# Kernel tuning notes

Measured on AMD Instinct MI355X. Metric: run time of the kernel, lower is better.

The kernel has to match this reference:

```python
import jax, jax.numpy as jnp
import numpy as np

N_EST = 5      # n_estimators
DEPTH = 6      # n_depth
LEAVES = 64    # 2 ** n_depth


def setup_inputs() -> dict:
    key = jax.random.key(0)
    ks = jax.random.split(key, 6)
    N, F, H, L, O = 131072, 256, 384, 64, 16
    X = jax.random.normal(ks[0], (N, F), jnp.float32)
    W1 = jax.random.normal(ks[1], (F, H), jnp.float32) / np.float32(np.sqrt(F))
    b1 = jnp.zeros((H,), jnp.float32)
    W2 = jax.random.normal(ks[2], (H, L), jnp.float32) / np.float32(np.sqrt(H))
    b2 = jnp.zeros((L,), jnp.float32)
    # phi[i] = random choice of n_leaves indices from arange(n_latent) without replacement
    phi = jnp.stack([jax.random.permutation(jax.random.fold_in(ks[3], i), L)[:LEAVES]
                     for i in range(N_EST)]).astype(jnp.int32)  # [E, 64]
    # pi: per-estimator leaf->label distributions (rows on the simplex, as after softmax updates)
    pi = jax.nn.softmax(jax.random.normal(ks[4], (N_EST, LEAVES, O), jnp.float32), axis=-1)
    return {"X": X, "W1": W1, "b1": b1, "W2": W2, "b2": b2, "phi": phi, "pi": pi}


def reference(X, W1, b1, W2, b2, phi, pi):
    # Backbone MLP: sigmoid -> sigmoid, as in keras.Sequential([Dense(h,'sigmoid'), Dense(l,'sigmoid')])
    h = jax.nn.sigmoid(X @ W1 + b1)          # [N, H]
    latent = jax.nn.sigmoid(h @ W2 + b2)     # [N, L]

    N = X.shape[0]
    E = phi.shape[0]
    d = latent[:, phi]                        # gather per estimator -> [N, E, 64]
    decisions = jnp.stack([d, 1.0 - d], axis=-1)  # [N, E, 64, 2] (go-left / go-right probs)

    # Soft tree routing: product of decision probs along each root->leaf path.
    # Level `lev` uses node indices [begin:begin+2**lev); index 0 is unused (matches TF code).
    mu = jnp.ones((N, E, 1, 1), X.dtype)
    begin = 1
    for lev in range(DEPTH):
        end = begin + 2 ** lev
        # reshape [N,E,k,2] -> [N,E,2k,1]; broadcast against [N,E,k_level,2] replaces tile(1,1,2)
        mu = mu.reshape(N, E, -1, 1) * decisions[:, :, begin:end, :]
        begin = end
    mu = mu.reshape(N, E, LEAVES)             # [N, E, 64] leaf arrival probabilities

    # predict: mean over estimators of mu_e @ pi_e
    return jnp.einsum('nel,elo->no', mu, pi) / E
```

## Files before the change

kernel.cpp:

```cpp
#include <hip/hip_runtime.h>
#include <hip/hip_bf16.h>
#include <stdint.h>

#define F_DIM 256
#define H_DIM 384
#define L_DIM 64
#define O_DIM 16
#define E_NUM 5
#define BM 64

#define XK_STRIDE 264
#define H_STRIDE 392
#define LAT_STRIDE 65
#define MU_STRIDE 328

#define LATT_OFF 50176
#define PHIS_OFF 66816
#define SMEM_BYTES 68096

typedef short bf16x8 __attribute__((ext_vector_type(8)));
typedef float f32x4 __attribute__((ext_vector_type(4)));

__device__ __forceinline__ unsigned short f2bf(float f) {
    union { float f; unsigned int u; } v; v.f = f;
    unsigned int u = v.u;
    return (unsigned short)((u + 0x7FFFu + ((u >> 16) & 1u)) >> 16);
}

__device__ __forceinline__ unsigned int pk2(float a, float b) {
#if defined(__has_builtin)
#if __has_builtin(__builtin_amdgcn_cvt_pk_bf16_f32)
    typedef __bf16 bf2 __attribute__((ext_vector_type(2)));
    bf2 p = __builtin_amdgcn_cvt_pk_bf16_f32(a, b);
    union { bf2 v; unsigned int u; } c; c.v = p;
    return c.u;
#else
    return (unsigned int)f2bf(a) | ((unsigned int)f2bf(b) << 16);
#endif
#else
    return (unsigned int)f2bf(a) | ((unsigned int)f2bf(b) << 16);
#endif
}

__device__ __forceinline__ uint2 cvt4(float4 v) {
    uint2 r; r.x = pk2(v.x, v.y); r.y = pk2(v.z, v.w); return r;
}

__device__ __forceinline__ float sigmoidf(float x) {
    return __builtin_amdgcn_rcpf(1.0f + __builtin_amdgcn_exp2f(-1.44269504088896f * x));
}

__global__ void prep_kernel(const float* __restrict__ W1, const float* __restrict__ W2,
                            const float* __restrict__ pi,
                            unsigned short* __restrict__ W1f,
                            unsigned short* __restrict__ W2f,
                            unsigned short* __restrict__ piTf) {
    __shared__ float tile[32][33];
    const int b = blockIdx.x;
    const int tid = threadIdx.x;
    const int tx = tid & 31, ty = tid >> 5;

    if (b < 120) {
        int ks, t0, nks;
        unsigned short* dst;
        if (b < 96) {
            const int fb = b / 12, hb = b % 12;
            #pragma unroll
            for (int s = 0; s < 32; s += 8)
                tile[ty + s][tx] = W1[(size_t)(fb * 32 + ty + s) * H_DIM + hb * 32 + tx];
            ks = fb; t0 = hb * 2; nks = 8; dst = W1f;
        } else {
            const int bb = b - 96, hb = bb / 2, lb = bb % 2;
            #pragma unroll
            for (int s = 0; s < 32; s += 8)
                tile[ty + s][tx] = W2[(size_t)(hb * 32 + ty + s) * L_DIM + lb * 32 + tx];
            ks = hb; t0 = lb * 2; nks = 12; dst = W2f;
        }
        __syncthreads();
        const int t_local = tid >> 7;
        const int r = (tid * 2) & 255;
        const int lane = r >> 2;
        const int e2b = r & 3;
        const int q = lane >> 4, c = lane & 15;
        const int f0 = q * 8 + e2b * 2;
        const int hl = t_local * 16 + c;
        uint2 v;
        v.x = pk2(tile[f0 + 0][hl], tile[f0 + 1][hl]);
        v.y = pk2(tile[f0 + 2][hl], tile[f0 + 3][hl]);
        const size_t off = ((size_t)((t0 + t_local) * nks + ks) * 64 + lane) * 8 + e2b * 2;
        *(uint2*)(dst + off) = v;
    } else {
        for (int i = tid; i < O_DIM * E_NUM * L_DIM; i += 256) {
            const int j = i & 7, lane = (i >> 3) & 63, ks = i >> 9;
            const int q = lane >> 4, c = lane & 15;
            const int k = ks * 32 + q * 8 + j;
            piTf[i] = f2bf(pi[k * O_DIM + c] * 0.2f);
        }
    }
}

__global__ __launch_bounds__(512, 4) void fused_kernel(
    const float* __restrict__ X,
    const unsigned short* __restrict__ W1f,
    const float* __restrict__ b1,
    const unsigned short* __restrict__ W2f,
    const float* __restrict__ b2,
    const int* __restrict__ phi,
    const unsigned short* __restrict__ piTf,
    float* __restrict__ out) {

    __shared__ __align__(16) unsigned char smem[SMEM_BYTES];
    unsigned short* Xs  = (unsigned short*)smem;
    unsigned short* Hs  = (unsigned short*)smem;
    unsigned short* mus = (unsigned short*)smem;
    float*          latT = (float*)(smem + LATT_OFF);
    int*            phis = (int*)(smem + PHIS_OFF);

    if (blockIdx.x < 512 && ((blockIdx.x >> 8) & 1)) {
        __builtin_amdgcn_s_sleep(127);
    }

    const int tid  = threadIdx.x;
    const int wave = tid >> 6;
    const int lane = tid & 63;
    const int q    = lane >> 4;
    const int c    = lane & 15;
    const int row0 = blockIdx.x * BM;

    if (tid < E_NUM * L_DIM) phis[tid] = phi[tid];

    {
        float4 t0[8];
        #pragma unroll
        for (int i = 0; i < 8; ++i)
            t0[i] = *(const float4*)(X + (size_t)(row0 + wave * 8 + i) * F_DIM + lane * 4);
        #pragma unroll
        for (int i = 0; i < 8; ++i)
            *(uint2*)&Xs[(wave * 8 + i) * XK_STRIDE + lane * 4] = cvt4(t0[i]);
    }

    bf16x8 af0[3];
    #pragma unroll
    for (int i = 0; i < 3; ++i)
        af0[i] = *(const bf16x8*)(W1f + ((size_t)((wave * 3 + i) * 8 + 0) * 64 + lane) * 8);

    __syncthreads();

    f32x4 acc[3][4];
    #pragma unroll
    for (int i = 0; i < 3; ++i)
        #pragma unroll
        for (int j = 0; j < 4; ++j)
            acc[i][j] = (f32x4){0.f, 0.f, 0.f, 0.f};

    {
        bf16x8 bf0[4];
        #pragma unroll
        for (int j = 0; j < 4; ++j)
            bf0[j] = *(const bf16x8*)&Xs[(j * 16 + c) * XK_STRIDE + q * 8];
        #pragma unroll
        for (int i = 0; i < 3; ++i)
            #pragma unroll
            for (int j = 0; j < 4; ++j)
                acc[i][j] = __builtin_amdgcn_mfma_f32_16x16x32_bf16(af0[i], bf0[j], acc[i][j], 0, 0, 0);
    }
    #pragma unroll 2
    for (int ks = 1; ks < 8; ++ks) {
        bf16x8 af[3];
        #pragma unroll
        for (int i = 0; i < 3; ++i)
            af[i] = *(const bf16x8*)(W1f + ((size_t)((wave * 3 + i) * 8 + ks) * 64 + lane) * 8);
        bf16x8 bf_[4];
        #pragma unroll
        for (int j = 0; j < 4; ++j)
            bf_[j] = *(const bf16x8*)&Xs[(j * 16 + c) * XK_STRIDE + ks * 32 + q * 8];
        #pragma unroll
        for (int i = 0; i < 3; ++i)
            #pragma unroll
            for (int j = 0; j < 4; ++j)
                acc[i][j] = __builtin_amdgcn_mfma_f32_16x16x32_bf16(af[i], bf_[j], acc[i][j], 0, 0, 0);
    }
    __syncthreads();

    const int lt = wave >> 1;
    bf16x8 wfrag[12];
    #pragma unroll
    for (int ks = 0; ks < 12; ++ks)
        wfrag[ks] = *(const bf16x8*)(W2f + ((size_t)(lt * 12 + ks) * 64 + lane) * 8);

    #pragma unroll
    for (int i = 0; i < 3; ++i) {
        const int n0 = wave * 48 + i * 16 + q * 4;
        float4 bv = *(const float4*)(b1 + n0);
        #pragma unroll
        for (int j = 0; j < 4; ++j) {
            const int m = j * 16 + c;
            uint2 h2;
            h2.x = pk2(sigmoidf(acc[i][j][0] + bv.x), sigmoidf(acc[i][j][1] + bv.y));
            h2.y = pk2(sigmoidf(acc[i][j][2] + bv.z), sigmoidf(acc[i][j][3] + bv.w));
            *(uint2*)&Hs[m * H_STRIDE + n0] = h2;
        }
    }
    __syncthreads();

    {
        const int mbase = (wave & 1) * 2;
        f32x4 acc2[2];
        acc2[0] = (f32x4){0.f, 0.f, 0.f, 0.f};
        acc2[1] = (f32x4){0.f, 0.f, 0.f, 0.f};
        #pragma unroll
        for (int ks = 0; ks < 12; ++ks) {
            #pragma unroll
            for (int j = 0; j < 2; ++j) {
                bf16x8 bf_ = *(const bf16x8*)&Hs[((mbase + j) * 16 + c) * H_STRIDE + ks * 32 + q * 8];
                acc2[j] = __builtin_amdgcn_mfma_f32_16x16x32_bf16(wfrag[ks], bf_, acc2[j], 0, 0, 0);
            }
        }
        const float4 b2v = *(const float4*)(b2 + lt * 16 + q * 4);
        #pragma unroll
        for (int j = 0; j < 2; ++j) {
            const int m = (mbase + j) * 16 + c;
            #pragma unroll
            for (int rg = 0; rg < 4; ++rg) {
                const int l = lt * 16 + q * 4 + rg;
                latT[l * LAT_STRIDE + m] = sigmoidf(acc2[j][rg] + ((const float*)&b2v)[rg]);
            }
        }
    }
    __syncthreads();

    bf16x8 pfrag[10];
    if (wave >= 5) {
        #pragma unroll
        for (int ks = 0; ks < 10; ++ks)
            pfrag[ks] = *(const bf16x8*)(piTf + ((size_t)ks * 64 + lane) * 8);
    }

    if (wave < E_NUM) {
        const int e = wave;
        const int r = lane;
        float mu[64];
        mu[0] = 1.0f;
        #pragma unroll
        for (int lev = 0; lev < 6; ++lev) {
            const int w = 1 << lev;
            #pragma unroll
            for (int i = w - 1; i >= 0; --i) {
                float d = latT[phis[e * 64 + w + i] * LAT_STRIDE + r];
                float m = mu[i];
                mu[2 * i + 1] = m - m * d;
                mu[2 * i]     = m * d;
            }
        }
        #pragma unroll
        for (int j8 = 0; j8 < 8; ++j8) {
            bf16x8 v;
            #pragma unroll
            for (int t = 0; t < 4; ++t) {
                unsigned int p = pk2(mu[j8 * 8 + 2 * t], mu[j8 * 8 + 2 * t + 1]);
                v[2 * t]     = (short)(p & 0xFFFF);
                v[2 * t + 1] = (short)(p >> 16);
            }
            *((bf16x8*)&mus[r * MU_STRIDE + e * 64 + j8 * 8]) = v;
        }
    }
    __syncthreads();

    if (wave >= 5) {
        for (int mt = wave - 5; mt < 4; mt += (wave == 5 ? 3 : 4)) {
            f32x4 acc3 = (f32x4){0.f, 0.f, 0.f, 0.f};
            #pragma unroll
            for (int ks = 0; ks < 10; ++ks) {
                bf16x8 af = *((const bf16x8*)&mus[(mt * 16 + c) * MU_STRIDE + ks * 32 + q * 8]);
                acc3 = __builtin_amdgcn_mfma_f32_16x16x32_bf16(af, pfrag[ks], acc3, 0, 0, 0);
            }
            #pragma unroll
            for (int rg = 0; rg < 4; ++rg) {
                const int m = mt * 16 + q * 4 + rg;
                out[(size_t)(row0 + m) * O_DIM + c] = acc3[rg];
            }
        }
    }
}

extern "C" void kernel_launch(void* const* d_in, const int* in_sizes, int n_in,
                              void* d_out, int out_size, void* d_ws, size_t ws_size,
                              hipStream_t stream) {
    (void)in_sizes; (void)n_in; (void)out_size; (void)ws_size;
    const float* X  = (const float*)d_in[0];
    const float* W1 = (const float*)d_in[1];
    const float* b1 = (const float*)d_in[2];
    const float* W2 = (const float*)d_in[3];
    const float* b2 = (const float*)d_in[4];
    const int*   phi = (const int*)d_in[5];
    const float* pi  = (const float*)d_in[6];
    float* out = (float*)d_out;

    unsigned short* W1f  = (unsigned short*)d_ws;
    unsigned short* W2f  = (unsigned short*)((char*)d_ws + 196608);
    unsigned short* piTf = (unsigned short*)((char*)d_ws + 196608 + 49152);

    prep_kernel<<<121, 256, 0, stream>>>(W1, W2, pi, W1f, W2f, piTf);

    const int nblocks = 131072 / BM;
    fused_kernel<<<nblocks, 512, 0, stream>>>(X, W1f, b1, W2f, b2, phi, piTf, out);
}
```

Before: 240.2 us.

## Split fused MLP-tree kernel into GEMM1 kernel and tail kernel via workspace

```diff
diff --git a/kernel.cpp b/kernel.cpp
--- a/kernel.cpp
+++ b/kernel.cpp
@@ -7,16 +7,11 @@
 #define L_DIM 64
 #define O_DIM 16
 #define E_NUM 5
-#define BM 64
 
 #define XK_STRIDE 264
 #define H_STRIDE 392
-#define LAT_STRIDE 65
-#define MU_STRIDE 328
-
-#define LATT_OFF 50176
-#define PHIS_OFF 66816
-#define SMEM_BYTES 68096
+#define LAT_STRIDE 33
+#define LAT_STRIDE64 65
 
 typedef short bf16x8 __attribute__((ext_vector_type(8)));
 typedef float f32x4 __attribute__((ext_vector_type(4)));
@@ -99,6 +94,214 @@
     }
 }
 
+__global__ __launch_bounds__(512, 4) void gemm1_kernel(
+    const float* __restrict__ X,
+    const unsigned short* __restrict__ W1f,
+    const float* __restrict__ b1,
+    unsigned short* __restrict__ Hf) {
+
+    __shared__ __align__(16) unsigned short Xs[64 * XK_STRIDE];
+
+    const int tid  = threadIdx.x;
+    const int wave = tid >> 6;
+    const int lane = tid & 63;
+    const int q    = lane >> 4;
+    const int c    = lane & 15;
+    const int row0 = blockIdx.x * 64;
+
+    {
+        float4 t0[8];
+        #pragma unroll
+        for (int i = 0; i < 8; ++i)
+            t0[i] = *(const float4*)(X + (size_t)(row0 + wave * 8 + i) * F_DIM + lane * 4);
+        #pragma unroll
+        for (int i = 0; i < 8; ++i)
+            *(uint2*)&Xs[(wave * 8 + i) * XK_STRIDE + lane * 4] = cvt4(t0[i]);
+    }
+
+    bf16x8 af0[3];
+    #pragma unroll
+    for (int i = 0; i < 3; ++i)
+        af0[i] = *(const bf16x8*)(W1f + ((size_t)((wave * 3 + i) * 8 + 0) * 64 + lane) * 8);
+
+    __syncthreads();
+
+    f32x4 acc[3][4];
+    #pragma unroll
+    for (int i = 0; i < 3; ++i)
+        #pragma unroll
+        for (int j = 0; j < 4; ++j)
+            acc[i][j] = (f32x4){0.f, 0.f, 0.f, 0.f};
+
+    {
+        bf16x8 bf0[4];
+        #pragma unroll
+        for (int j = 0; j < 4; ++j)
+            bf0[j] = *(const bf16x8*)&Xs[(j * 16 + c) * XK_STRIDE + q * 8];
+        #pragma unroll
+        for (int i = 0; i < 3; ++i)
+            #pragma unroll
+            for (int j = 0; j < 4; ++j)
+                acc[i][j] = __builtin_amdgcn_mfma_f32_16x16x32_bf16(af0[i], bf0[j], acc[i][j], 0, 0, 0);
+    }
+    #pragma unroll 2
+    for (int ks = 1; ks < 8; ++ks) {
+        bf16x8 af[3];
+        #pragma unroll
+        for (int i = 0; i < 3; ++i)
+            af[i] = *(const bf16x8*)(W1f + ((size_t)((wave * 3 + i) * 8 + ks) * 64 + lane) * 8);
+        bf16x8 bf_[4];
+        #pragma unroll
+        for (int j = 0; j < 4; ++j)
+            bf_[j] = *(const bf16x8*)&Xs[(j * 16 + c) * XK_STRIDE + ks * 32 + q * 8];
+        #pragma unroll
+        for (int i = 0; i < 3; ++i)
+            #pragma unroll
+            for (int j = 0; j < 4; ++j)
+                acc[i][j] = __builtin_amdgcn_mfma_f32_16x16x32_bf16(af[i], bf_[j], acc[i][j], 0, 0, 0);
+    }
+
+    const int mtGbase = blockIdx.x * 4;
+    #pragma unroll
+    for (int i = 0; i < 3; ++i) {
+        const int colbase = wave * 48 + i * 16 + q * 4;
+        const int ks2 = colbase >> 5;
+        const int qp  = (colbase >> 3) & 3;
+        const int jj0 = colbase & 7;
+        const float4 bv = *(const float4*)(b1 + colbase);
+        #pragma unroll
+        for (int j = 0; j < 4; ++j) {
+            uint2 h2;
+            h2.x = pk2(sigmoidf(acc[i][j][0] + bv.x), sigmoidf(acc[i][j][1] + bv.y));
+            h2.y = pk2(sigmoidf(acc[i][j][2] + bv.z), sigmoidf(acc[i][j][3] + bv.w));
+            *(uint2*)(Hf + ((size_t)((mtGbase + j) * 12 + ks2) * 64 + qp * 16 + c) * 8 + jj0) = h2;
+        }
+    }
+}
+
+__global__ __launch_bounds__(256, 4) void tail_kernel(
+    const unsigned short* __restrict__ Hf,
+    const unsigned short* __restrict__ W2f,
+    const float* __restrict__ b2,
+    const int* __restrict__ phi,
+    const unsigned short* __restrict__ piTf,
+    float* __restrict__ out) {
+
+    __shared__ __align__(16) unsigned char smem[34304];
+    unsigned short* HsL  = (unsigned short*)smem;
+    unsigned short* musf = (unsigned short*)smem;
+    float*          latT = (float*)(smem + 24576);
+    int*            phis = (int*)(smem + 33024);
+
+    const int tid  = threadIdx.x;
+    const int wave = tid >> 6;
+    const int lane = tid & 63;
+    const int q    = lane >> 4;
+    const int c    = lane & 15;
+    const int row0 = blockIdx.x * 32;
+
+    uint4 hv[6];
+    #pragma unroll
+    for (int s = 0; s < 6; ++s)
+        hv[s] = *(const uint4*)(Hf + (size_t)blockIdx.x * 12288 + s * 2048 + tid * 8);
+
+    for (int idx = tid; idx < E_NUM * L_DIM; idx += 256) phis[idx] = phi[idx];
+
+    bf16x8 wfrag[12];
+    #pragma unroll
+    for (int ks = 0; ks < 12; ++ks)
+        wfrag[ks] = *(const bf16x8*)(W2f + ((size_t)(wave * 12 + ks) * 64 + lane) * 8);
+
+    #pragma unroll
+    for (int s = 0; s < 6; ++s)
+        *(uint4*)&HsL[s * 2048 + tid * 8] = hv[s];
+
+    __syncthreads();
+
+    {
+        f32x4 acc2[2];
+        acc2[0] = (f32x4){0.f, 0.f, 0.f, 0.f};
+        acc2[1] = (f32x4){0.f, 0.f, 0.f, 0.f};
+        #pragma unroll
+        for (int ks = 0; ks < 12; ++ks) {
+            #pragma unroll
+            for (int j = 0; j < 2; ++j) {
+                bf16x8 bf_ = *(const bf16x8*)&HsL[((j * 12 + ks) * 64 + lane) * 8];
+                acc2[j] = __builtin_amdgcn_mfma_f32_16x16x32_bf16(wfrag[ks], bf_, acc2[j], 0, 0, 0);
+            }
+        }
+        const int lb = wave * 16;
+        const float4 b2v = *(const float4*)(b2 + lb + q * 4);
+        #pragma unroll
+        for (int j = 0; j < 2; ++j) {
+            const int m = j * 16 + c;
+            #pragma unroll
+            for (int rg = 0; rg < 4; ++rg) {
+                const int l = lb + q * 4 + rg;
+                latT[l * LAT_STRIDE + m] = sigmoidf(acc2[j][rg] + ((const float*)&b2v)[rg]);
+            }
+        }
+    }
+    __syncthreads();
+
+    {
+        const int r = lane & 31;
+        const int e = wave * 2 + (lane >> 5);
+        if (e < E_NUM) {
+            float mu[64];
+            mu[0] = 1.0f;
+            #pragma unroll
+            for (int lev = 0; lev < 6; ++lev) {
+                const int w = 1 << lev;
+                #pragma unroll
+                for (int i = w - 1; i >= 0; --i) {
+                    float d = latT[phis[e * 64 + w + i] * LAT_STRIDE + r];
+                    float m = mu[i];
+                    mu[2 * i + 1] = m - m * d;
+                    mu[2 * i]     = m * d;
+                }
+            }
+            const int mt = r >> 4;
+            const int rc = r & 15;
+            #pragma unroll
+            for (int j8 = 0; j8 < 8; ++j8) {
+                bf16x8 v;
+                #pragma unroll
+                for (int t = 0; t < 4; ++t) {
+                    unsigned int p = pk2(mu[j8 * 8 + 2 * t], mu[j8 * 8 + 2 * t + 1]);
+                    v[2 * t]     = (short)(p & 0xFFFF);
+                    v[2 * t + 1] = (short)(p >> 16);
+                }
+                const int ksf = 2 * e + (j8 >> 2);
+                const int qf  = j8 & 3;
+                *((bf16x8*)&musf[((mt * 10 + ksf) * 64 + qf * 16 + rc) * 8]) = v;
+            }
+        }
+    }
+    __syncthreads();
+
+    if (wave >= 2) {
+        const int mt = wave - 2;
+        bf16x8 pfrag[10];
+        #pragma unroll
+        for (int ks = 0; ks < 10; ++ks)
+            pfrag[ks] = *(const bf16x8*)(piTf + ((size_t)ks * 64 + lane) * 8);
+        f32x4 acc3 = (f32x4){0.f, 0.f, 0.f, 0.f};
+        #pragma unroll
+        for (int ks = 0; ks < 10; ++ks) {
+            bf16x8 af = *((const bf16x8*)&musf[((mt * 10 + ks) * 64 + lane) * 8]);
+            acc3 = __builtin_amdgcn_mfma_f32_16x16x32_bf16(af, pfrag[ks], acc3, 0, 0, 0);
+        }
+        #pragma unroll
+        for (int rg = 0; rg < 4; ++rg) {
+            const int m = mt * 16 + q * 4 + rg;
+            out[(size_t)(row0 + m) * O_DIM + c] = acc3[rg];
+        }
+    }
+}
+
+#define FB_LATT_OFF 50176
+#define FB_PHIS_OFF 66816
 __global__ __launch_bounds__(512, 4) void fused_kernel(
     const float* __restrict__ X,
     const unsigned short* __restrict__ W1f,
@@ -109,23 +312,20 @@
     const unsigned short* __restrict__ piTf,
     float* __restrict__ out) {
 
-    __shared__ __align__(16) unsigned char smem[SMEM_BYTES];
-    unsigned short* Xs  = (unsigned short*)smem;
-    unsigned short* Hs  = (unsigned short*)smem;
-    unsigned short* mus = (unsigned short*)smem;
-    float*          latT = (float*)(smem + LATT_OFF);
-    int*            phis = (int*)(smem + PHIS_OFF);
-
-    if (blockIdx.x < 512 && ((blockIdx.x >> 8) & 1)) {
-        __builtin_amdgcn_s_sleep(127);
-    }
+    __shared__ __align__(16) unsigned char smem[68096];
+    unsigned short* Xs   = (unsigned short*)smem;
+    unsigned short* Hs   = (unsigned short*)smem;
+    unsigned short* mus  = (unsigned short*)smem;
+    float*          latT = (float*)(smem + FB_LATT_OFF);
+    int*            phis = (int*)(smem + FB_PHIS_OFF);
+    #define MU_STRIDE 328
 
     const int tid  = threadIdx.x;
     const int wave = tid >> 6;
     const int lane = tid & 63;
     const int q    = lane >> 4;
     const int c    = lane & 15;
-    const int row0 = blockIdx.x * BM;
+    const int row0 = blockIdx.x * 64;
 
     if (tid < E_NUM * L_DIM) phis[tid] = phi[tid];
 
@@ -138,12 +338,10 @@
         for (int i = 0; i < 8; ++i)
             *(uint2*)&Xs[(wave * 8 + i) * XK_STRIDE + lane * 4] = cvt4(t0[i]);
     }
-
     bf16x8 af0[3];
     #pragma unroll
     for (int i = 0; i < 3; ++i)
         af0[i] = *(const bf16x8*)(W1f + ((size_t)((wave * 3 + i) * 8 + 0) * 64 + lane) * 8);
-
     __syncthreads();
 
     f32x4 acc[3][4];
@@ -152,7 +350,6 @@
         #pragma unroll
         for (int j = 0; j < 4; ++j)
             acc[i][j] = (f32x4){0.f, 0.f, 0.f, 0.f};
-
     {
         bf16x8 bf0[4];
         #pragma unroll
@@ -223,7 +420,7 @@
             #pragma unroll
             for (int rg = 0; rg < 4; ++rg) {
                 const int l = lt * 16 + q * 4 + rg;
-                latT[l * LAT_STRIDE + m] = sigmoidf(acc2[j][rg] + ((const float*)&b2v)[rg]);
+                latT[l * LAT_STRIDE64 + m] = sigmoidf(acc2[j][rg] + ((const float*)&b2v)[rg]);
             }
         }
     }
@@ -235,7 +432,6 @@
         for (int ks = 0; ks < 10; ++ks)
             pfrag[ks] = *(const bf16x8*)(piTf + ((size_t)ks * 64 + lane) * 8);
     }
-
     if (wave < E_NUM) {
         const int e = wave;
         const int r = lane;
@@ -246,7 +442,7 @@
             const int w = 1 << lev;
             #pragma unroll
             for (int i = w - 1; i >= 0; --i) {
-                float d = latT[phis[e * 64 + w + i] * LAT_STRIDE + r];
+                float d = latT[phis[e * 64 + w + i] * LAT_STRIDE64 + r];
                 float m = mu[i];
                 mu[2 * i + 1] = m - m * d;
                 mu[2 * i]     = m * d;
@@ -286,7 +482,7 @@
 extern "C" void kernel_launch(void* const* d_in, const int* in_sizes, int n_in,
                               void* d_out, int out_size, void* d_ws, size_t ws_size,
                               hipStream_t stream) {
-    (void)in_sizes; (void)n_in; (void)out_size; (void)ws_size;
+    (void)in_sizes; (void)n_in; (void)out_size;
     const float* X  = (const float*)d_in[0];
     const float* W1 = (const float*)d_in[1];
     const float* b1 = (const float*)d_in[2];
@@ -299,9 +495,15 @@
     unsigned short* W1f  = (unsigned short*)d_ws;
     unsigned short* W2f  = (unsigned short*)((char*)d_ws + 196608);
     unsigned short* piTf = (unsigned short*)((char*)d_ws + 196608 + 49152);
+    unsigned short* Hf   = (unsigned short*)((char*)d_ws + 262144);
 
     prep_kernel<<<121, 256, 0, stream>>>(W1, W2, pi, W1f, W2f, piTf);
 
-    const int nblocks = 131072 / BM;
-    fused_kernel<<<nblocks, 512, 0, stream>>>(X, W1f, b1, W2f, b2, phi, piTf, out);
-}
+    const size_t need = 262144ull + 100663296ull;
+    if (ws_size >= need) {
+        gemm1_kernel<<<131072 / 64, 512, 0, stream>>>(X, W1f, b1, Hf);
+        tail_kernel<<<131072 / 32, 256, 0, stream>>>(Hf, W2f, b2, phi, piTf, out);
+    } else {
+        fused_kernel<<<131072 / 64, 512, 0, stream>>>(X, W1f, b1, W2f, b2, phi, piTf, out);
+    }
+}
```

Result: slower. 274.4 us (+14.2%).

## Make fused kernel persistent with register-prefetched next X tile

Applied to the files above, without the earlier changes.

```diff
diff --git a/kernel.cpp b/kernel.cpp
--- a/kernel.cpp
+++ b/kernel.cpp
@@ -7,16 +7,18 @@
 #define L_DIM 64
 #define O_DIM 16
 #define E_NUM 5
-#define BM 64
 
 #define XK_STRIDE 264
 #define H_STRIDE 392
-#define LAT_STRIDE 65
+#define LAT_STRIDE64 65
 #define MU_STRIDE 328
 
 #define LATT_OFF 50176
 #define PHIS_OFF 66816
 #define SMEM_BYTES 68096
+
+#define N_TILES 2048
+#define NBLOCKS 512
 
 typedef short bf16x8 __attribute__((ext_vector_type(8)));
 typedef float f32x4 __attribute__((ext_vector_type(4)));
@@ -110,124 +112,25 @@
     float* __restrict__ out) {
 
     __shared__ __align__(16) unsigned char smem[SMEM_BYTES];
-    unsigned short* Xs  = (unsigned short*)smem;
-    unsigned short* Hs  = (unsigned short*)smem;
-    unsigned short* mus = (unsigned short*)smem;
+    unsigned short* Xs   = (unsigned short*)smem;
+    unsigned short* Hs   = (unsigned short*)smem;
+    unsigned short* mus  = (unsigned short*)smem;
     float*          latT = (float*)(smem + LATT_OFF);
     int*            phis = (int*)(smem + PHIS_OFF);
-
-    if (blockIdx.x < 512 && ((blockIdx.x >> 8) & 1)) {
-        __builtin_amdgcn_s_sleep(127);
-    }
 
     const int tid  = threadIdx.x;
     const int wave = tid >> 6;
     const int lane = tid & 63;
     const int q    = lane >> 4;
     const int c    = lane & 15;
-    const int row0 = blockIdx.x * BM;
 
     if (tid < E_NUM * L_DIM) phis[tid] = phi[tid];
-
-    {
-        float4 t0[8];
-        #pragma unroll
-        for (int i = 0; i < 8; ++i)
-            t0[i] = *(const float4*)(X + (size_t)(row0 + wave * 8 + i) * F_DIM + lane * 4);
-        #pragma unroll
-        for (int i = 0; i < 8; ++i)
-            *(uint2*)&Xs[(wave * 8 + i) * XK_STRIDE + lane * 4] = cvt4(t0[i]);
-    }
-
-    bf16x8 af0[3];
-    #pragma unroll
-    for (int i = 0; i < 3; ++i)
-        af0[i] = *(const bf16x8*)(W1f + ((size_t)((wave * 3 + i) * 8 + 0) * 64 + lane) * 8);
-
-    __syncthreads();
-
-    f32x4 acc[3][4];
-    #pragma unroll
-    for (int i = 0; i < 3; ++i)
-        #pragma unroll
-        for (int j = 0; j < 4; ++j)
-            acc[i][j] = (f32x4){0.f, 0.f, 0.f, 0.f};
-
-    {
-        bf16x8 bf0[4];
-        #pragma unroll
-        for (int j = 0; j < 4; ++j)
-            bf0[j] = *(const bf16x8*)&Xs[(j * 16 + c) * XK_STRIDE + q * 8];
-        #pragma unroll
-        for (int i = 0; i < 3; ++i)
-            #pragma unroll
-            for (int j = 0; j < 4; ++j)
-                acc[i][j] = __builtin_amdgcn_mfma_f32_16x16x32_bf16(af0[i], bf0[j], acc[i][j], 0, 0, 0);
-    }
-    #pragma unroll 2
-    for (int ks = 1; ks < 8; ++ks) {
-        bf16x8 af[3];
-        #pragma unroll
-        for (int i = 0; i < 3; ++i)
-            af[i] = *(const bf16x8*)(W1f + ((size_t)((wave * 3 + i) * 8 + ks) * 64 + lane) * 8);
-        bf16x8 bf_[4];
-        #pragma unroll
-        for (int j = 0; j < 4; ++j)
-            bf_[j] = *(const bf16x8*)&Xs[(j * 16 + c) * XK_STRIDE + ks * 32 + q * 8];
-        #pragma unroll
-        for (int i = 0; i < 3; ++i)
-            #pragma unroll
-            for (int j = 0; j < 4; ++j)
-                acc[i][j] = __builtin_amdgcn_mfma_f32_16x16x32_bf16(af[i], bf_[j], acc[i][j], 0, 0, 0);
-    }
-    __syncthreads();
 
     const int lt = wave >> 1;
     bf16x8 wfrag[12];
     #pragma unroll
     for (int ks = 0; ks < 12; ++ks)
         wfrag[ks] = *(const bf16x8*)(W2f + ((size_t)(lt * 12 + ks) * 64 + lane) * 8);
-
-    #pragma unroll
-    for (int i = 0; i < 3; ++i) {
-        const int n0 = wave * 48 + i * 16 + q * 4;
-        float4 bv = *(const float4*)(b1 + n0);
-        #pragma unroll
-        for (int j = 0; j < 4; ++j) {
-            const int m = j * 16 + c;
-            uint2 h2;
-            h2.x = pk2(sigmoidf(acc[i][j][0] + bv.x), sigmoidf(acc[i][j][1] + bv.y));
-            h2.y = pk2(sigmoidf(acc[i][j][2] + bv.z), sigmoidf(acc[i][j][3] + bv.w));
-            *(uint2*)&Hs[m * H_STRIDE + n0] = h2;
-        }
-    }
-    __syncthreads();
-
-    {
-        const int mbase = (wave & 1) * 2;
-        f32x4 acc2[2];
-        acc2[0] = (f32x4){0.f, 0.f, 0.f, 0.f};
-        acc2[1] = (f32x4){0.f, 0.f, 0.f, 0.f};
-        #pragma unroll
-        for (int ks = 0; ks < 12; ++ks) {
-            #pragma unroll
-            for (int j = 0; j < 2; ++j) {
-                bf16x8 bf_ = *(const bf16x8*)&Hs[((mbase + j) * 16 + c) * H_STRIDE + ks * 32 + q * 8];
-                acc2[j] = __builtin_amdgcn_mfma_f32_16x16x32_bf16(wfrag[ks], bf_, acc2[j], 0, 0, 0);
-            }
-        }
-        const float4 b2v = *(const float4*)(b2 + lt * 16 + q * 4);
-        #pragma unroll
-        for (int j = 0; j < 2; ++j) {
-            const int m = (mbase + j) * 16 + c;
-            #pragma unroll
-            for (int rg = 0; rg < 4; ++rg) {
-                const int l = lt * 16 + q * 4 + rg;
-                latT[l * LAT_STRIDE + m] = sigmoidf(acc2[j][rg] + ((const float*)&b2v)[rg]);
-            }
-        }
-    }
-    __syncthreads();
 
     bf16x8 pfrag[10];
     if (wave >= 5) {
@@ -236,50 +139,162 @@
             pfrag[ks] = *(const bf16x8*)(piTf + ((size_t)ks * 64 + lane) * 8);
     }
 
-    if (wave < E_NUM) {
-        const int e = wave;
-        const int r = lane;
-        float mu[64];
-        mu[0] = 1.0f;
+    bf16x8 af0[3];
+    #pragma unroll
+    for (int i = 0; i < 3; ++i)
+        af0[i] = *(const bf16x8*)(W1f + ((size_t)((wave * 3 + i) * 8 + 0) * 64 + lane) * 8);
+
+    float4 b1v[3];
+    #pragma unroll
+    for (int i = 0; i < 3; ++i)
+        b1v[i] = *(const float4*)(b1 + wave * 48 + i * 16 + q * 4);
+    const float4 b2v = *(const float4*)(b2 + lt * 16 + q * 4);
+
+    int tile = blockIdx.x;
+    float4 t0[8];
+    #pragma unroll
+    for (int i = 0; i < 8; ++i)
+        t0[i] = *(const float4*)(X + (size_t)(tile * 64 + wave * 8 + i) * F_DIM + lane * 4);
+
+    while (tile < N_TILES) {
+        const int row0 = tile * 64;
+
         #pragma unroll
-        for (int lev = 0; lev < 6; ++lev) {
-            const int w = 1 << lev;
-            #pragma unroll
-            for (int i = w - 1; i >= 0; --i) {
-                float d = latT[phis[e * 64 + w + i] * LAT_STRIDE + r];
-                float m = mu[i];
-                mu[2 * i + 1] = m - m * d;
-                mu[2 * i]     = m * d;
-            }
-        }
+        for (int i = 0; i < 8; ++i)
+            *(uint2*)&Xs[(wave * 8 + i) * XK_STRIDE + lane * 4] = cvt4(t0[i]);
+
+        const int nxt = tile + NBLOCKS;
+        if (nxt < N_TILES) {
+            #pragma unroll
+            for (int i = 0; i < 8; ++i)
+                t0[i] = *(const float4*)(X + (size_t)(nxt * 64 + wave * 8 + i) * F_DIM + lane * 4);
+        }
+        __syncthreads();
+
+        f32x4 acc[3][4];
         #pragma unroll
-        for (int j8 = 0; j8 < 8; ++j8) {
-            bf16x8 v;
-            #pragma unroll
-            for (int t = 0; t < 4; ++t) {
-                unsigned int p = pk2(mu[j8 * 8 + 2 * t], mu[j8 * 8 + 2 * t + 1]);
-                v[2 * t]     = (short)(p & 0xFFFF);
-                v[2 * t + 1] = (short)(p >> 16);
-            }
-            *((bf16x8*)&mus[r * MU_STRIDE + e * 64 + j8 * 8]) = v;
-        }
-    }
-    __syncthreads();
-
-    if (wave >= 5) {
-        for (int mt = wave - 5; mt < 4; mt += (wave == 5 ? 3 : 4)) {
-            f32x4 acc3 = (f32x4){0.f, 0.f, 0.f, 0.f};
-            #pragma unroll
-            for (int ks = 0; ks < 10; ++ks) {
-                bf16x8 af = *((const bf16x8*)&mus[(mt * 16 + c) * MU_STRIDE + ks * 32 + q * 8]);
-                acc3 = __builtin_amdgcn_mfma_f32_16x16x32_bf16(af, pfrag[ks], acc3, 0, 0, 0);
-            }
-            #pragma unroll
-            for (int rg = 0; rg < 4; ++rg) {
-                const int m = mt * 16 + q * 4 + rg;
-                out[(size_t)(row0 + m) * O_DIM + c] = acc3[rg];
-            }
-        }
+        for (int i = 0; i < 3; ++i)
+            #pragma unroll
+            for (int j = 0; j < 4; ++j)
+                acc[i][j] = (f32x4){0.f, 0.f, 0.f, 0.f};
+
+        {
+            bf16x8 bf0[4];
+            #pragma unroll
+            for (int j = 0; j < 4; ++j)
+                bf0[j] = *(const bf16x8*)&Xs[(j * 16 + c) * XK_STRIDE + q * 8];
+            #pragma unroll
+            for (int i = 0; i < 3; ++i)
+                #pragma unroll
+                for (int j = 0; j < 4; ++j)
+                    acc[i][j] = __builtin_amdgcn_mfma_f32_16x16x32_bf16(af0[i], bf0[j], acc[i][j], 0, 0, 0);
+        }
+        #pragma unroll 2
+        for (int ks = 1; ks < 8; ++ks) {
+            bf16x8 af[3];
+            #pragma unroll
+            for (int i = 0; i < 3; ++i)
+                af[i] = *(const bf16x8*)(W1f + ((size_t)((wave * 3 + i) * 8 + ks) * 64 + lane) * 8);
+            bf16x8 bf_[4];
+            #pragma unroll
+            for (int j = 0; j < 4; ++j)
+                bf_[j] = *(const bf16x8*)&Xs[(j * 16 + c) * XK_STRIDE + ks * 32 + q * 8];
+            #pragma unroll
+            for (int i = 0; i < 3; ++i)
+                #pragma unroll
+                for (int j = 0; j < 4; ++j)
+                    acc[i][j] = __builtin_amdgcn_mfma_f32_16x16x32_bf16(af[i], bf_[j], acc[i][j], 0, 0, 0);
+        }
+        __syncthreads();
+
+        #pragma unroll
+        for (int i = 0; i < 3; ++i) {
+            const int n0 = wave * 48 + i * 16 + q * 4;
+            const float4 bv = b1v[i];
+            #pragma unroll
+            for (int j = 0; j < 4; ++j) {
+                const int m = j * 16 + c;
+                uint2 h2;
+                h2.x = pk2(sigmoidf(acc[i][j][0] + bv.x), sigmoidf(acc[i][j][1] + bv.y));
+                h2.y = pk2(sigmoidf(acc[i][j][2] + bv.z), sigmoidf(acc[i][j][3] + bv.w));
+                *(uint2*)&Hs[m * H_STRIDE + n0] = h2;
+            }
+        }
+        __syncthreads();
+
+        {
+            const int mbase = (wave & 1) * 2;
+            f32x4 acc2[2];
+            acc2[0] = (f32x4){0.f, 0.f, 0.f, 0.f};
+            acc2[1] = (f32x4){0.f, 0.f, 0.f, 0.f};
+            #pragma unroll
+            for (int ks = 0; ks < 12; ++ks) {
+                #pragma unroll
+                for (int j = 0; j < 2; ++j) {
+                    bf16x8 bf_ = *(const bf16x8*)&Hs[((mbase + j) * 16 + c) * H_STRIDE + ks * 32 + q * 8];
+                    acc2[j] = __builtin_amdgcn_mfma_f32_16x16x32_bf16(wfrag[ks], bf_, acc2[j], 0, 0, 0);
+                }
+            }
+            #pragma unroll
+            for (int j = 0; j < 2; ++j) {
+                const int m = (mbase + j) * 16 + c;
+                #pragma unroll
+                for (int rg = 0; rg < 4; ++rg) {
+                    const int l = lt * 16 + q * 4 + rg;
+                    latT[l * LAT_STRIDE64 + m] = sigmoidf(acc2[j][rg] + ((const float*)&b2v)[rg]);
+                }
+            }
+        }
+        __syncthreads();
+
+        if (wave < E_NUM) {
+            const int e = wave;
+            const int r = lane;
+            float mu[64];
+            mu[0] = 1.0f;
+            #pragma unroll
+            for (int lev = 0; lev < 6; ++lev) {
+                const int w = 1 << lev;
+                #pragma unroll
+                for (int i = w - 1; i >= 0; --i) {
+                    float d = latT[phis[e * 64 + w + i] * LAT_STRIDE64 + r];
+                    float m = mu[i];
+                    mu[2 * i + 1] = m - m * d;
+                    mu[2 * i]     = m * d;
+                }
+            }
+            #pragma unroll
+            for (int j8 = 0; j8 < 8; ++j8) {
+                bf16x8 v;
+                #pragma unroll
+                for (int t = 0; t < 4; ++t) {
+                    unsigned int p = pk2(mu[j8 * 8 + 2 * t], mu[j8 * 8 + 2 * t + 1]);
+                    v[2 * t]     = (short)(p & 0xFFFF);
+                    v[2 * t + 1] = (short)(p >> 16);
+                }
+                *((bf16x8*)&mus[r * MU_STRIDE + e * 64 + j8 * 8]) = v;
+            }
+        }
+        __syncthreads();
+
+        if (wave >= 5) {
+            for (int mt = wave - 5; mt < 4; mt += (wave == 5 ? 3 : 4)) {
+                f32x4 acc3 = (f32x4){0.f, 0.f, 0.f, 0.f};
+                #pragma unroll
+                for (int ks = 0; ks < 10; ++ks) {
+                    bf16x8 af = *((const bf16x8*)&mus[(mt * 16 + c) * MU_STRIDE + ks * 32 + q * 8]);
+                    acc3 = __builtin_amdgcn_mfma_f32_16x16x32_bf16(af, pfrag[ks], acc3, 0, 0, 0);
+                }
+                #pragma unroll
+                for (int rg = 0; rg < 4; ++rg) {
+                    const int m = mt * 16 + q * 4 + rg;
+                    out[(size_t)(row0 + m) * O_DIM + c] = acc3[rg];
+                }
+            }
+        }
+        __syncthreads();
+
+        tile = nxt;
     }
 }
 
@@ -301,7 +316,5 @@
     unsigned short* piTf = (unsigned short*)((char*)d_ws + 196608 + 49152);
 
     prep_kernel<<<121, 256, 0, stream>>>(W1, W2, pi, W1f, W2f, piTf);
-
-    const int nblocks = 131072 / BM;
-    fused_kernel<<<nblocks, 512, 0, stream>>>(X, W1f, b1, W2f, b2, phi, piTf, out);
-}
+    fused_kernel<<<NBLOCKS, 512, 0, stream>>>(X, W1f, b1, W2f, b2, phi, piTf, out);
+}
```

After: 443.5 us. +84.6%, slower.
